# Optimization experiments

Hardware: AMD Instinct MI355X
Metric: run time of the kernel (lower is better)

The kernel has to match this reference:

```python
import jax, jax.numpy as jnp
import numpy as np

EMBED = 2048
N_HEAD = 32
N_KV = 8
HEAD_DIM = 64
GROUP = N_HEAD // N_KV


def _rope_tables(seq_len, head_dim):
    inv_freq = 1.0 / (10000.0 ** (jnp.arange(0, head_dim, 2, dtype=jnp.float32) / head_dim))
    ang = jnp.arange(seq_len, dtype=jnp.float32)[:, None] * inv_freq[None, :]  # [S, D/2]
    ang = jnp.concatenate([ang, ang], axis=-1)  # [S, D]
    return jnp.cos(ang), jnp.sin(ang)


def apply_rope(x, cos, sin, offset=0):
    # x: [B, H, S, D]
    S, D = x.shape[2], x.shape[3]
    x1, x2 = x[..., : D // 2], x[..., D // 2 :]
    c = cos[offset : offset + S][None, None]
    s = sin[offset : offset + S][None, None]
    rotated = jnp.concatenate([-x2, x1], axis=-1)
    return (x * c + rotated * s).astype(x.dtype)


def setup_inputs() -> dict:
    key = jax.random.key(0)
    kx, kq, kk, kv, ko = jax.random.split(key, 5)
    B, S = 2, 2048
    x = jax.random.normal(kx, (B, S, EMBED), dtype=jnp.float32)
    mask = jnp.triu(jnp.ones((S, S), dtype=bool), k=1)  # causal: True = masked
    cos, sin = _rope_tables(S, HEAD_DIM)
    std = 0.02
    Wq = jax.random.normal(kq, (EMBED, EMBED), dtype=jnp.float32) * std
    Wk = jax.random.normal(kk, (EMBED, N_KV * HEAD_DIM), dtype=jnp.float32) * std
    Wv = jax.random.normal(kv, (EMBED, N_KV * HEAD_DIM), dtype=jnp.float32) * std
    Wo = jax.random.normal(ko, (EMBED, EMBED), dtype=jnp.float32) * std
    return {"x": x, "mask": mask, "cos": cos, "sin": sin,
            "Wq": Wq, "Wk": Wk, "Wv": Wv, "Wo": Wo}


def reference(x, mask, cos, sin, Wq, Wk, Wv, Wo):
    B, S, E = x.shape
    # projections (no bias)
    q = (x @ Wq).reshape(B, S, N_HEAD, HEAD_DIM).transpose(0, 2, 1, 3)  # [B,H,S,D]
    k = (x @ Wk).reshape(B, S, N_KV, HEAD_DIM).transpose(0, 2, 1, 3)    # [B,G,S,D]
    v = (x @ Wv).reshape(B, S, N_KV, HEAD_DIM).transpose(0, 2, 1, 3)    # [B,G,S,D]
    q = apply_rope(q, cos, sin, offset=0)
    k = apply_rope(k, cos, sin, offset=0)
    next_k, next_v = k, v  # kv cache to return
    # GQA: head h uses kv group h // GROUP; avoid repeat_interleave via reshape
    qg = q.reshape(B, N_KV, GROUP, S, HEAD_DIM)
    scores = jnp.einsum('bgjsd,bgtd->bgjst', qg, k) / np.float32(np.sqrt(HEAD_DIM))
    scores = jnp.where(mask[None, None, None], -jnp.inf, scores)
    attn = jax.nn.softmax(scores, axis=-1)
    out = jnp.einsum('bgjst,bgtd->bgjsd', attn, v)          # [B,G,group,S,D]
    out = out.reshape(B, N_HEAD, S, HEAD_DIM).transpose(0, 2, 1, 3).reshape(B, S, E)
    return out @ Wo, next_k, next_v
```

## Files before the change

### kernel.cpp

```cpp
#include <hip/hip_runtime.h>
#include <hip/hip_bf16.h>
#include <math.h>

#define NH 32
#define NKV 8
#define HD 64
#define B_ 2
#define S_ 2048
#define E_ 2048
#define M_ 4096

typedef unsigned short ushort_t;
typedef __attribute__((ext_vector_type(8))) short short8;
typedef __attribute__((ext_vector_type(4))) short short4v;
typedef __attribute__((ext_vector_type(4))) float floatx4;

__device__ inline unsigned short f2bf(float f) {
  unsigned int u = __float_as_uint(f);
  return (unsigned short)((u + 0x7FFFu + ((u >> 16) & 1u)) >> 16);
}

__device__ inline float fexp2(float x) {
  float r;
  asm("v_exp_f32 %0, %1" : "=v"(r) : "v"(x));
  return r;
}

__device__ inline void ld_lds16(const void* g, void* l) {
  __builtin_amdgcn_global_load_lds((__attribute__((address_space(1))) void*)g,
                                   (__attribute__((address_space(3))) void*)l, 16, 0, 0);
}

__device__ inline void transp32(const float* __restrict__ in, ushort_t* __restrict__ out,
                                int R, int C, int bx, int by, int tid, float (*tile)[33]) {
  int c0 = bx * 32, r0 = by * 32;
  int x = tid & 31, y0 = tid >> 5;
  for (int i = 0; i < 4; i++) {
    int r = y0 + i * 8;
    tile[r][x] = in[(size_t)(r0 + r) * C + c0 + x];
  }
  __syncthreads();
  for (int i = 0; i < 4; i++) {
    int r = y0 + i * 8;
    out[(size_t)(c0 + r) * R + r0 + x] = f2bf(tile[x][r]);
  }
}

__global__ __launch_bounds__(256) void prep(const float* __restrict__ x,
                                            ushort_t* __restrict__ xb,
                                            const float* __restrict__ Wq,
                                            const float* __restrict__ Wk,
                                            const float* __restrict__ Wv,
                                            const float* __restrict__ Wo,
                                            ushort_t* __restrict__ WT,
                                            ushort_t* __restrict__ WoT) {
  __shared__ float tile[32][33];
  int bid = blockIdx.x, tid = threadIdx.x;
  if (bid < 4096) {
    size_t i = ((size_t)bid * 256 + tid) * 8;
    float4 a = *(const float4*)(x + i);
    float4 b = *(const float4*)(x + i + 4);
    short8 o;
    o[0] = (short)f2bf(a.x); o[1] = (short)f2bf(a.y);
    o[2] = (short)f2bf(a.z); o[3] = (short)f2bf(a.w);
    o[4] = (short)f2bf(b.x); o[5] = (short)f2bf(b.y);
    o[6] = (short)f2bf(b.z); o[7] = (short)f2bf(b.w);
    *(short8*)(xb + i) = o;
    return;
  }
  bid -= 4096;
  if (bid < 4096) { transp32(Wq, WT, 2048, 2048, bid & 63, bid >> 6, tid, tile); return; }
  bid -= 4096;
  if (bid < 1024) { transp32(Wk, WT + 2048 * 2048, 2048, 512, bid & 15, bid >> 4, tid, tile); return; }
  bid -= 1024;
  if (bid < 1024) { transp32(Wv, WT + 2560 * 2048, 2048, 512, bid & 15, bid >> 4, tid, tile); return; }
  bid -= 1024;
  transp32(Wo, WoT, 2048, 2048, bid & 63, bid >> 6, tid, tile);
}

__global__ __launch_bounds__(512) void gemm_qkv(const ushort_t* __restrict__ xb,
                                                const ushort_t* __restrict__ WT,
                                                ushort_t* __restrict__ qbf,
                                                float* __restrict__ outk,
                                                ushort_t* __restrict__ kbf,
                                                float* __restrict__ outv,
                                                ushort_t* __restrict__ vt,
                                                const float* __restrict__ cosP,
                                                const float* __restrict__ sinP) {
  __shared__ __align__(16) ushort_t L8[2][2][2][128][64];
  char* Lb = (char*)L8;
  int bid = blockIdx.x;
  int xcd = bid & 7, ii = bid >> 3;
  int mg = xcd >> 1, ng = xcd & 1;
  int m0 = (mg * 4 + ii / 6) * 256;
  int n0 = (ng * 6 + ii % 6) * 256;
  int tid = threadIdx.x;
  int w8 = tid >> 6, lane = tid & 63;
  int wrq = w8 >> 1, wcq = w8 & 1;
  int lr = lane & 15, quad = lane >> 4;
  int sx = lr & 7;
  int srow = w8 * 16 + (lane >> 3);
  int schunk = (lane & 7) ^ (lane >> 3);
  const char* abase = (const char*)(xb + (size_t)m0 * 2048);
  const char* bbase = (const char*)(WT + (size_t)n0 * 2048);
  floatx4 acc[4][2][4] = {};

#define STG(T, U)                                                                        \
  do {                                                                                   \
    const int mat_ = (U)&1, half_ = (U) >> 1;                                            \
    const char* sp = (mat_ ? bbase : abase) + (size_t)(half_ * 128 + srow) * 4096 +      \
                     (size_t)(T)*128 + schunk * 16;                                      \
    char* dp = Lb + (((T)&1) * 65536) + mat_ * 32768 + half_ * 16384 + w8 * 2048;        \
    ld_lds16(sp, dp);                                                                    \
    ld_lds16(sp + (size_t)8 * 4096, dp + 1024);                                          \
  } while (0)

#define PH(T, P, MH_, NH_, WAITS, DOSTAGE)                                               \
  do {                                                                                   \
    asm volatile(WAITS ::: "memory");                                                    \
    const char* Ab_ = Lb + (((T)&1) * 65536) + (MH_)*16384;                              \
    const char* Bb_ = Lb + (((T)&1) * 65536) + 32768 + (NH_)*16384;                      \
    short8 af_[2][2], bf_[4][2];                                                         \
    _Pragma("unroll") for (int i = 0; i < 2; i++) {                                      \
      size_t rb = (size_t)(wrq * 32 + i * 16 + lr) * 128;                                \
      _Pragma("unroll") for (int ks = 0; ks < 2; ks++)                                   \
          af_[i][ks] = *(const short8*)(Ab_ + rb + (((ks * 4 + quad) ^ sx) << 4));       \
    }                                                                                    \
    _Pragma("unroll") for (int j = 0; j < 4; j++) {                                      \
      size_t rb = (size_t)(wcq * 64 + j * 16 + lr) * 128;                                \
      _Pragma("unroll") for (int ks = 0; ks < 2; ks++)                                   \
          bf_[j][ks] = *(const short8*)(Bb_ + rb + (((ks * 4 + quad) ^ sx) << 4));       \
    }                                                                                    \
    if (DOSTAGE) STG((T) + 1, P);                                                        \
    __builtin_amdgcn_s_setprio(1);                                                       \
    _Pragma("unroll") for (int i = 0; i < 2; i++) _Pragma("unroll") for (int j = 0;      \
                                                                         j < 4; j++) {  \
      acc[P][i][j] =                                                                     \
          __builtin_amdgcn_mfma_f32_16x16x32_bf16(af_[i][0], bf_[j][0], acc[P][i][j],    \
                                                  0, 0, 0);                              \
      acc[P][i][j] =                                                                     \
          __builtin_amdgcn_mfma_f32_16x16x32_bf16(af_[i][1], bf_[j][1], acc[P][i][j],    \
                                                  0, 0, 0);                              \
    }                                                                                    \
    __builtin_amdgcn_s_setprio(0);                                                       \
  } while (0)

  STG(0, 0); STG(0, 1); STG(0, 2); STG(0, 3);

  for (int kt = 0; kt < 31; kt++) {
    PH(kt, 0, 0, 0, "s_waitcnt vmcnt(4)\n\ts_barrier", 1);
    PH(kt, 1, 1, 0, "s_waitcnt vmcnt(4)\n\ts_barrier", 1);
    PH(kt, 2, 1, 1, "s_waitcnt vmcnt(4)\n\ts_barrier", 1);
    PH(kt, 3, 0, 1, "s_barrier", 1);
  }
  PH(31, 0, 0, 0, "s_waitcnt vmcnt(4)\n\ts_barrier", 0);
  PH(31, 1, 1, 0, "s_waitcnt vmcnt(2)\n\ts_barrier", 0);
  PH(31, 2, 1, 1, "s_waitcnt vmcnt(0)\n\ts_barrier", 0);
  PH(31, 3, 0, 1, "s_barrier", 0);
#undef STG
#undef PH

  const int MHs[4] = {0, 1, 1, 0}, NHs[4] = {0, 0, 1, 1};
  if (n0 < 2048) {
    const float QS = 0.125f * 1.4426950408889634f;
#pragma unroll
    for (int p = 0; p < 4; p++)
#pragma unroll
      for (int i = 0; i < 2; i++)
#pragma unroll
        for (int j = 0; j < 2; j++) {
          int d = j * 16 + lr;
#pragma unroll
          for (int r = 0; r < 4; r++) {
            int row = m0 + MHs[p] * 128 + wrq * 32 + i * 16 + quad * 4 + r;
            int s = row & (S_ - 1);
            float c = cosP[s * 64 + d], sn = sinP[s * 64 + d];
            float x1 = acc[p][i][j][r], x2 = acc[p][i][j + 2][r];
            size_t oo = (size_t)row * 2048 + n0 + NHs[p] * 128 + wcq * 64 + d;
            qbf[oo] = f2bf((x1 * c - x2 * sn) * QS);
            qbf[oo + 32] = f2bf((x2 * c + x1 * sn) * QS);
          }
        }
  } else if (n0 < 2560) {
#pragma unroll
    for (int p = 0; p < 4; p++) {
      int h = ((n0 - 2048) >> 6) + NHs[p] * 2 + wcq;
#pragma unroll
      for (int i = 0; i < 2; i++)
#pragma unroll
        for (int j = 0; j < 2; j++) {
          int d = j * 16 + lr;
#pragma unroll
          for (int r = 0; r < 4; r++) {
            int row = m0 + MHs[p] * 128 + wrq * 32 + i * 16 + quad * 4 + r;
            int s = row & (S_ - 1), b = row >> 11;
            float c = cosP[s * 64 + d], sn = sinP[s * 64 + d];
            float x1 = acc[p][i][j][r], x2 = acc[p][i][j + 2][r];
            float y1 = x1 * c - x2 * sn, y2 = x2 * c + x1 * sn;
            size_t rowb = ((size_t)(b * NKV + h) * S_ + s) * 64;
            int xr = (s & 7) << 3;
            outk[rowb + d] = y1; outk[rowb + d + 32] = y2;
            kbf[rowb + (d ^ xr)] = f2bf(y1);
            kbf[rowb + ((d + 32) ^ xr)] = f2bf(y2);
          }
        }
    }
  } else {
#pragma unroll
    for (int p = 0; p < 4; p++) {
      int h = ((n0 - 2560) >> 6) + NHs[p] * 2 + wcq;
#pragma unroll
      for (int i = 0; i < 2; i++)
#pragma unroll
        for (int j = 0; j < 4; j++) {
          int d = j * 16 + lr;
          int row0 = m0 + MHs[p] * 128 + wrq * 32 + i * 16 + quad * 4;
          int s0 = row0 & (S_ - 1), b = row0 >> 11;
#pragma unroll
          for (int r = 0; r < 4; r++)
            outv[((size_t)(b * NKV + h) * S_ + s0 + r) * 64 + d] = acc[p][i][j][r];
          int tt = s0 >> 6, s4 = s0 & 63;
          short4v u;
          u[0] = (short)f2bf(acc[p][i][j][0]); u[1] = (short)f2bf(acc[p][i][j][1]);
          u[2] = (short)f2bf(acc[p][i][j][2]); u[3] = (short)f2bf(acc[p][i][j][3]);
          *(short4v*)(vt + ((size_t)(b * NKV + h) * 32 + tt) * 4096 + d * 64 +
                      (s4 ^ ((d & 7) << 3))) = u;
        }
    }
  }
}

__device__ __forceinline__ void gemm128_core(const ushort_t* __restrict__ Ag,
                                             const ushort_t* __restrict__ Bg,
                                             floatx4 (&acc)[4][4]) {
  __shared__ __align__(16) ushort_t As[2][128][64];
  __shared__ __align__(16) ushort_t Bs[2][128][64];
  int tid = threadIdx.x;
  int w = tid >> 6, lane = tid & 63;
  int wm = (w >> 1) * 64, wn = (w & 1) * 64;
  int lr = lane & 15, quad = lane >> 4;
  int sx = lr & 7;
  char* Asb = (char*)As;
  char* Bsb = (char*)Bs;

  size_t so[4];
#pragma unroll
  for (int s = 0; s < 4; s++)
    so[s] = (size_t)(w * 32 + s * 8 + (lane >> 3)) * 4096 + (size_t)(((lane & 7) ^ (lane >> 3)) * 16);
  const char* abase = (const char*)Ag;
  const char* bbase = (const char*)Bg;

#define STAGE128(buf, kt)                                          \
  do {                                                             \
    size_t ko = (size_t)(kt) * 128;                                \
    char* Ad = Asb + (buf) * 16384 + w * 4096;                     \
    char* Bd = Bsb + (buf) * 16384 + w * 4096;                     \
    _Pragma("unroll") for (int s = 0; s < 4; s++) {                \
      ld_lds16(abase + so[s] + ko, Ad + s * 1024);                 \
      ld_lds16(bbase + so[s] + ko, Bd + s * 1024);                 \
    }                                                              \
  } while (0)

  STAGE128(0, 0);
  __syncthreads();

  int cur = 0;
  for (int kt = 0; kt < 32; kt++) {
    if (kt < 31) STAGE128(cur ^ 1, kt + 1);
    const char* Ab = Asb + cur * 16384;
    const char* Bb = Bsb + cur * 16384;
    short8 af[4][2], bfr[4][2];
#pragma unroll
    for (int i = 0; i < 4; i++) {
      size_t rb = (size_t)(wm + i * 16 + lr) * 128;
#pragma unroll
      for (int ks = 0; ks < 2; ks++)
        af[i][ks] = *(const short8*)(Ab + rb + (((ks * 4 + quad) ^ sx) << 4));
    }
#pragma unroll
    for (int j = 0; j < 4; j++) {
      size_t rb = (size_t)(wn + j * 16 + lr) * 128;
#pragma unroll
      for (int ks = 0; ks < 2; ks++)
        bfr[j][ks] = *(const short8*)(Bb + rb + (((ks * 4 + quad) ^ sx) << 4));
    }
#pragma unroll
    for (int i = 0; i < 4; i++)
#pragma unroll
      for (int j = 0; j < 4; j++) {
        acc[i][j] = __builtin_amdgcn_mfma_f32_16x16x32_bf16(af[i][0], bfr[j][0], acc[i][j], 0, 0, 0);
        acc[i][j] = __builtin_amdgcn_mfma_f32_16x16x32_bf16(af[i][1], bfr[j][1], acc[i][j], 0, 0, 0);
      }
    __syncthreads();
    cur ^= 1;
  }
#undef STAGE128
}

__global__ __launch_bounds__(256) void gemm_o(const ushort_t* __restrict__ ctx,
                                              const ushort_t* __restrict__ WoT,
                                              float* __restrict__ y) {
  int o = blockIdx.y * 16 + blockIdx.x;
  int xcd = o & 7, i = o >> 3;
  int mg = xcd >> 1, ng = xcd & 1;
  int m0 = (mg * 8 + (i >> 3)) * 128;
  int n0 = (ng * 8 + (i & 7)) * 128;
  int tid = threadIdx.x;
  int w = tid >> 6, lane = tid & 63;
  int wm = (w >> 1) * 64, wn = (w & 1) * 64;
  int lr = lane & 15, quad = lane >> 4;

  floatx4 acc[4][4] = {};
  gemm128_core(ctx + (size_t)m0 * 2048, WoT + (size_t)n0 * 2048, acc);

#pragma unroll
  for (int i2 = 0; i2 < 4; i2++)
#pragma unroll
    for (int j = 0; j < 4; j++) {
      int row = m0 + wm + i2 * 16 + quad * 4;
      int col = n0 + wn + j * 16 + lr;
#pragma unroll
      for (int r = 0; r < 4; r++)
        y[(size_t)(row + r) * 2048 + col] = acc[i2][j][r];
    }
}

__global__ __launch_bounds__(256, 3) void attn2(ushort_t* __restrict__ q,
                                                const ushort_t* __restrict__ k,
                                                const ushort_t* __restrict__ vt) {
  __shared__ __align__(16) ushort_t KV[2][2][64][64];
  __shared__ __align__(16) ushort_t Ps[4][2][16][64];
  int bh = blockIdx.x;
  int qi = 15 - blockIdx.y;
  int b = bh >> 5, h = bh & 31, g = h >> 2;
  int tid = threadIdx.x;
  int w = tid >> 6, lane = tid & 63;
  int lr = lane & 15, quad = lane >> 4;

  int qg0 = qi * 128 + w * 16 + lr;
  int qg1 = qg0 + 64;
  short8 a00, a01, a10, a11;
  {
    const ushort_t* qp0 = q + ((size_t)(b * S_ + qg0) * NH + h) * HD;
    const ushort_t* qp1 = q + ((size_t)(b * S_ + qg1) * NH + h) * HD;
    a00 = *(const short8*)(qp0 + quad * 8);
    a01 = *(const short8*)(qp0 + 32 + quad * 8);
    a10 = *(const short8*)(qp1 + quad * 8);
    a11 = *(const short8*)(qp1 + 32 + quad * 8);
  }
  floatx4 od0[4] = {}, od1[4] = {};
  float mi0 = -INFINITY, li0 = 0.f, mi1 = -INFINITY, li1 = 0.f;

  const char* ksrc = (const char*)(k + (size_t)(b * NKV + g) * S_ * HD) + w * 2048 + lane * 16;
  const char* vsrc = (const char*)(vt + (size_t)(b * NKV + g) * S_ * HD) + w * 2048 + lane * 16;
  char* dB = (char*)&KV[0][0][0][0] + w * 2048;

  int sw = (lr & 7) << 4;
  int ro0 = (quad * 16) ^ sw;
  int ro1 = (64 + quad * 16) ^ sw;
  char* Pw = (char*)&Ps[0][0][0][0] + w * 4096;

  ld_lds16(ksrc, dB);
  ld_lds16(ksrc + 1024, dB + 1024);
  ld_lds16(vsrc, dB + 8192);
  ld_lds16(vsrc + 1024, dB + 8192 + 1024);
  asm volatile("s_waitcnt vmcnt(0)" ::: "memory");
  __syncthreads();

  int T = 2 * qi + 2;
  int cur = 0;
  for (int t = 0; t < T; t++) {
    if (t + 1 < T) {
      const char* kn = ksrc + (size_t)(t + 1) * 8192;
      const char* vn = vsrc + (size_t)(t + 1) * 8192;
      char* d = dB + (cur ^ 1) * 16384;
      ld_lds16(kn, d); ld_lds16(kn + 1024, d + 1024);
      ld_lds16(vn, d + 8192); ld_lds16(vn + 1024, d + 8192 + 1024);
    }
    const char* Kb = (const char*)&KV[cur][0][0][0];
    const char* Vb = (const char*)&KV[cur][1][0][0];
    bool dq0 = (t == 2 * qi);
    bool skip0 = (t == 2 * qi + 1);
    if (!skip0) {
      floatx4 sc[4];
      __builtin_amdgcn_s_setprio(1);
#pragma unroll
      for (int kn = 0; kn < 4; kn++) {
        short8 k0 = *(const short8*)(Kb + (kn * 16 + lr) * 128 + ro0);
        short8 k1 = *(const short8*)(Kb + (kn * 16 + lr) * 128 + ro1);
        floatx4 c = {};
        c = __builtin_amdgcn_mfma_f32_16x16x32_bf16(k0, a00, c, 0, 0, 0);
        c = __builtin_amdgcn_mfma_f32_16x16x32_bf16(k1, a01, c, 0, 0, 0);
        sc[kn] = c;
      }
      __builtin_amdgcn_s_setprio(0);
      float pv[16];
#pragma unroll
      for (int kn = 0; kn < 4; kn++)
#pragma unroll
        for (int r = 0; r < 4; r++) pv[kn * 4 + r] = sc[kn][r];
      if (dq0) {
#pragma unroll
        for (int e = 0; e < 16; e++) {
          int kg = t * 64 + (e >> 2) * 16 + quad * 4 + (e & 3);
          if (kg > qg0) pv[e] = -INFINITY;
        }
      }
      float mx = pv[0];
#pragma unroll
      for (int e = 1; e < 16; e++) mx = fmaxf(mx, pv[e]);
      mx = fmaxf(mx, __shfl_xor(mx, 16));
      mx = fmaxf(mx, __shfl_xor(mx, 32));
      if (__any(mx > mi0 + 11.5f)) {
        float mn = fmaxf(mi0, mx);
        float al = fexp2(mi0 - mn);
        li0 *= al;
#pragma unroll
        for (int dn = 0; dn < 4; dn++) {
          od0[dn][0] *= al; od0[dn][1] *= al; od0[dn][2] *= al; od0[dn][3] *= al;
        }
        mi0 = mn;
      }
      float ps = 0.f;
#pragma unroll
      for (int e = 0; e < 16; e++) {
        pv[e] = fexp2(pv[e] - mi0);
        ps += pv[e];
      }
      ps += __shfl_xor(ps, 16);
      ps += __shfl_xor(ps, 32);
      li0 += ps;
#pragma unroll
      for (int kn = 0; kn < 4; kn++) {
        unsigned int u0, u1;
        asm("v_cvt_pk_bf16_f32 %0, %1, %2" : "=v"(u0) : "v"(pv[kn * 4 + 0]), "v"(pv[kn * 4 + 1]));
        asm("v_cvt_pk_bf16_f32 %0, %1, %2" : "=v"(u1) : "v"(pv[kn * 4 + 2]), "v"(pv[kn * 4 + 3]));
        uint2 uu; uu.x = u0; uu.y = u1;
        *(uint2*)(Pw + lr * 128 + ((kn * 32 + quad * 8) ^ sw)) = uu;
      }
    }
    {
      floatx4 sc[4];
      __builtin_amdgcn_s_setprio(1);
#pragma unroll
      for (int kn = 0; kn < 4; kn++) {
        short8 k0 = *(const short8*)(Kb + (kn * 16 + lr) * 128 + ro0);
        short8 k1 = *(const short8*)(Kb + (kn * 16 + lr) * 128 + ro1);
        floatx4 c = {};
        c = __builtin_amdgcn_mfma_f32_16x16x32_bf16(k0, a10, c, 0, 0, 0);
        c = __builtin_amdgcn_mfma_f32_16x16x32_bf16(k1, a11, c, 0, 0, 0);
        sc[kn] = c;
      }
      __builtin_amdgcn_s_setprio(0);
      float pv[16];
#pragma unroll
      for (int kn = 0; kn < 4; kn++)
#pragma unroll
        for (int r = 0; r < 4; r++) pv[kn * 4 + r] = sc[kn][r];
      if (skip0) {
#pragma unroll
        for (int e = 0; e < 16; e++) {
          int kg = t * 64 + (e >> 2) * 16 + quad * 4 + (e & 3);
          if (kg > qg1) pv[e] = -INFINITY;
        }
      }
      float mx = pv[0];
#pragma unroll
      for (int e = 1; e < 16; e++) mx = fmaxf(mx, pv[e]);
      mx = fmaxf(mx, __shfl_xor(mx, 16));
      mx = fmaxf(mx, __shfl_xor(mx, 32));
      if (__any(mx > mi1 + 11.5f)) {
        float mn = fmaxf(mi1, mx);
        float al = fexp2(mi1 - mn);
        li1 *= al;
#pragma unroll
        for (int dn = 0; dn < 4; dn++) {
          od1[dn][0] *= al; od1[dn][1] *= al; od1[dn][2] *= al; od1[dn][3] *= al;
        }
        mi1 = mn;
      }
      float ps = 0.f;
#pragma unroll
      for (int e = 0; e < 16; e++) {
        pv[e] = fexp2(pv[e] - mi1);
        ps += pv[e];
      }
      ps += __shfl_xor(ps, 16);
      ps += __shfl_xor(ps, 32);
      li1 += ps;
#pragma unroll
      for (int kn = 0; kn < 4; kn++) {
        unsigned int u0, u1;
        asm("v_cvt_pk_bf16_f32 %0, %1, %2" : "=v"(u0) : "v"(pv[kn * 4 + 0]), "v"(pv[kn * 4 + 1]));
        asm("v_cvt_pk_bf16_f32 %0, %1, %2" : "=v"(u1) : "v"(pv[kn * 4 + 2]), "v"(pv[kn * 4 + 3]));
        uint2 uu; uu.x = u0; uu.y = u1;
        *(uint2*)(Pw + 2048 + lr * 128 + ((kn * 32 + quad * 8) ^ sw)) = uu;
      }
    }
    __builtin_amdgcn_s_setprio(1);
    if (!skip0) {
      short8 pb0 = *(const short8*)(Pw + lr * 128 + ro0);
      short8 pb1 = *(const short8*)(Pw + lr * 128 + ro1);
#pragma unroll
      for (int dn = 0; dn < 4; dn++) {
        short8 va = *(const short8*)(Vb + (dn * 16 + lr) * 128 + ro0);
        short8 vb = *(const short8*)(Vb + (dn * 16 + lr) * 128 + ro1);
        od0[dn] = __builtin_amdgcn_mfma_f32_16x16x32_bf16(va, pb0, od0[dn], 0, 0, 0);
        od0[dn] = __builtin_amdgcn_mfma_f32_16x16x32_bf16(vb, pb1, od0[dn], 0, 0, 0);
      }
    }
    {
      short8 pb0 = *(const short8*)(Pw + 2048 + lr * 128 + ro0);
      short8 pb1 = *(const short8*)(Pw + 2048 + lr * 128 + ro1);
#pragma unroll
      for (int dn = 0; dn < 4; dn++) {
        short8 va = *(const short8*)(Vb + (dn * 16 + lr) * 128 + ro0);
        short8 vb = *(const short8*)(Vb + (dn * 16 + lr) * 128 + ro1);
        od1[dn] = __builtin_amdgcn_mfma_f32_16x16x32_bf16(va, pb0, od1[dn], 0, 0, 0);
        od1[dn] = __builtin_amdgcn_mfma_f32_16x16x32_bf16(vb, pb1, od1[dn], 0, 0, 0);
      }
    }
    __builtin_amdgcn_s_setprio(0);
    asm volatile("s_waitcnt vmcnt(0)" ::: "memory");
    __syncthreads();
    cur ^= 1;
  }
  float inv0 = 1.f / li0, inv1 = 1.f / li1;
  ushort_t* outp0 = q + ((size_t)(b * S_ + qg0) * NH + h) * HD;
  ushort_t* outp1 = q + ((size_t)(b * S_ + qg1) * NH + h) * HD;
#pragma unroll
  for (int dn = 0; dn < 4; dn++) {
    short4v u;
    u[0] = (short)f2bf(od0[dn][0] * inv0); u[1] = (short)f2bf(od0[dn][1] * inv0);
    u[2] = (short)f2bf(od0[dn][2] * inv0); u[3] = (short)f2bf(od0[dn][3] * inv0);
    *(short4v*)(outp0 + dn * 16 + quad * 4) = u;
    short4v v;
    v[0] = (short)f2bf(od1[dn][0] * inv1); v[1] = (short)f2bf(od1[dn][1] * inv1);
    v[2] = (short)f2bf(od1[dn][2] * inv1); v[3] = (short)f2bf(od1[dn][3] * inv1);
    *(short4v*)(outp1 + dn * 16 + quad * 4) = v;
  }
}

extern "C" void kernel_launch(void* const* d_in, const int* in_sizes, int n_in,
                              void* d_out, int out_size, void* d_ws, size_t ws_size,
                              hipStream_t stream) {
  const float* x = (const float*)d_in[0];
  const float* cosT = (const float*)d_in[2];
  const float* sinT = (const float*)d_in[3];
  const float* Wq = (const float*)d_in[4];
  const float* Wk = (const float*)d_in[5];
  const float* Wv = (const float*)d_in[6];
  const float* Wo = (const float*)d_in[7];

  char* ws = (char*)d_ws;
  ushort_t* WT = (ushort_t*)(ws);
  ushort_t* WoT = (ushort_t*)(ws + 12582912);
  ushort_t* xb = (ushort_t*)(ws + 20971520);
  ushort_t* qbf = (ushort_t*)(ws + 37748736);
  ushort_t* kbf = (ushort_t*)(ws + 54525952);
  ushort_t* vt = (ushort_t*)(ws + 58720256);

  float* y = (float*)d_out;
  float* outk = y + (size_t)M_ * E_;
  float* outv = outk + (size_t)B_ * NKV * S_ * HD;

  prep<<<dim3(14336), 256, 0, stream>>>(x, xb, Wq, Wk, Wv, Wo, WT, WoT);

  gemm_qkv<<<dim3(192), 512, 0, stream>>>(xb, WT, qbf, outk, kbf, outv, vt, cosT, sinT);

  attn2<<<dim3(64, 16), 256, 0, stream>>>(qbf, kbf, vt);

  gemm_o<<<dim3(16, 32), 256, 0, stream>>>(qbf, WoT, y);
}
```

Measured before the change: 303.9 us.

## Restructure output GEMM into 128x256 tiles with 8 waves and phased pipelining

The output projection GEMM moves from 128x128 tiles with 4 waves to 128x256 tiles with 8 waves, launched as 256 blocks with an XCD-aware mapping. The K loop is split into four quadrant phases. Each phase loads one slice of the next tile through hand-placed vmcnt waits and barriers, raising MFMA priority with setprio so loads overlap compute. This aims to improve data reuse and latency hiding, at the cost of fewer blocks (256 on the GPU), a larger LDS footprint, and fragile manual waitcnt bookkeeping.

```diff
diff --git a/kernel.cpp b/kernel.cpp
--- a/kernel.cpp
+++ b/kernel.cpp
@@ -230,99 +230,106 @@
   }
 }
 
-__device__ __forceinline__ void gemm128_core(const ushort_t* __restrict__ Ag,
-                                             const ushort_t* __restrict__ Bg,
-                                             floatx4 (&acc)[4][4]) {
+__global__ __launch_bounds__(512) void gemm_o(const ushort_t* __restrict__ ctx,
+                                              const ushort_t* __restrict__ WoT,
+                                              float* __restrict__ y) {
   __shared__ __align__(16) ushort_t As[2][128][64];
-  __shared__ __align__(16) ushort_t Bs[2][128][64];
+  __shared__ __align__(16) ushort_t Bs[2][256][64];
+  char* Ab0 = (char*)As;
+  char* Bb0 = (char*)Bs;
+  int bid = blockIdx.x;
+  int xcd = bid & 7, ii = bid >> 3;
+  int mg = xcd >> 1, ng = xcd & 1;
+  int m0 = (mg * 8 + (ii >> 2)) * 128;
+  int n0 = (ng * 4 + (ii & 3)) * 256;
   int tid = threadIdx.x;
-  int w = tid >> 6, lane = tid & 63;
-  int wm = (w >> 1) * 64, wn = (w & 1) * 64;
+  int w8 = tid >> 6, lane = tid & 63;
+  int wrq = w8 >> 2, wcq = w8 & 3;
   int lr = lane & 15, quad = lane >> 4;
   int sx = lr & 7;
-  char* Asb = (char*)As;
-  char* Bsb = (char*)Bs;
-
-  size_t so[4];
-#pragma unroll
-  for (int s = 0; s < 4; s++)
-    so[s] = (size_t)(w * 32 + s * 8 + (lane >> 3)) * 4096 + (size_t)(((lane & 7) ^ (lane >> 3)) * 16);
-  const char* abase = (const char*)Ag;
-  const char* bbase = (const char*)Bg;
-
-#define STAGE128(buf, kt)                                          \
-  do {                                                             \
-    size_t ko = (size_t)(kt) * 128;                                \
-    char* Ad = Asb + (buf) * 16384 + w * 4096;                     \
-    char* Bd = Bsb + (buf) * 16384 + w * 4096;                     \
-    _Pragma("unroll") for (int s = 0; s < 4; s++) {                \
-      ld_lds16(abase + so[s] + ko, Ad + s * 1024);                 \
-      ld_lds16(bbase + so[s] + ko, Bd + s * 1024);                 \
-    }                                                              \
+  int lrow = lane >> 3;
+  int schunk = (lane & 7) ^ lrow;
+  const char* abase = (const char*)(ctx + (size_t)m0 * 2048);
+  const char* bbase = (const char*)(WoT + (size_t)n0 * 2048);
+  floatx4 acc[4][2][2] = {};
+
+#define STG_O(T, U)                                                                      \
+  do {                                                                                   \
+    size_t ko = (size_t)(T)*128;                                                         \
+    if (((U)&1) == 0) {                               \
+      const int half_ = (U) >> 1;                                                        \
+      const char* sp = abase + (size_t)(half_ * 64 + w8 * 8 + lrow) * 4096 + ko +        \
+                       schunk * 16;                                                      \
+      char* dp = Ab0 + (((T)&1) * 16384) + half_ * 8192 + w8 * 1024;                     \
+      ld_lds16(sp, dp);                                                                  \
+    } else {                                        \
+      const int half_ = (U) >> 1;                                                        \
+      const char* sp = bbase + (size_t)(half_ * 128 + w8 * 16 + lrow) * 4096 + ko +      \
+                       schunk * 16;                                                      \
+      char* dp = Bb0 + (((T)&1) * 32768) + half_ * 16384 + w8 * 2048;                    \
+      ld_lds16(sp, dp);                                                                  \
+      ld_lds16(sp + (size_t)8 * 4096, dp + 1024);                                        \
+    }                                                                                    \
   } while (0)
 
-  STAGE128(0, 0);
-  __syncthreads();
-
-  int cur = 0;
-  for (int kt = 0; kt < 32; kt++) {
-    if (kt < 31) STAGE128(cur ^ 1, kt + 1);
-    const char* Ab = Asb + cur * 16384;
-    const char* Bb = Bsb + cur * 16384;
-    short8 af[4][2], bfr[4][2];
-#pragma unroll
-    for (int i = 0; i < 4; i++) {
-      size_t rb = (size_t)(wm + i * 16 + lr) * 128;
-#pragma unroll
-      for (int ks = 0; ks < 2; ks++)
-        af[i][ks] = *(const short8*)(Ab + rb + (((ks * 4 + quad) ^ sx) << 4));
-    }
-#pragma unroll
-    for (int j = 0; j < 4; j++) {
-      size_t rb = (size_t)(wn + j * 16 + lr) * 128;
-#pragma unroll
-      for (int ks = 0; ks < 2; ks++)
-        bfr[j][ks] = *(const short8*)(Bb + rb + (((ks * 4 + quad) ^ sx) << 4));
-    }
-#pragma unroll
-    for (int i = 0; i < 4; i++)
-#pragma unroll
-      for (int j = 0; j < 4; j++) {
-        acc[i][j] = __builtin_amdgcn_mfma_f32_16x16x32_bf16(af[i][0], bfr[j][0], acc[i][j], 0, 0, 0);
-        acc[i][j] = __builtin_amdgcn_mfma_f32_16x16x32_bf16(af[i][1], bfr[j][1], acc[i][j], 0, 0, 0);
-      }
-    __syncthreads();
-    cur ^= 1;
-  }
-#undef STAGE128
-}
-
-__global__ __launch_bounds__(256) void gemm_o(const ushort_t* __restrict__ ctx,
-                                              const ushort_t* __restrict__ WoT,
-                                              float* __restrict__ y) {
-  int o = blockIdx.y * 16 + blockIdx.x;
-  int xcd = o & 7, i = o >> 3;
-  int mg = xcd >> 1, ng = xcd & 1;
-  int m0 = (mg * 8 + (i >> 3)) * 128;
-  int n0 = (ng * 8 + (i & 7)) * 128;
-  int tid = threadIdx.x;
-  int w = tid >> 6, lane = tid & 63;
-  int wm = (w >> 1) * 64, wn = (w & 1) * 64;
-  int lr = lane & 15, quad = lane >> 4;
-
-  floatx4 acc[4][4] = {};
-  gemm128_core(ctx + (size_t)m0 * 2048, WoT + (size_t)n0 * 2048, acc);
-
-#pragma unroll
-  for (int i2 = 0; i2 < 4; i2++)
-#pragma unroll
-    for (int j = 0; j < 4; j++) {
-      int row = m0 + wm + i2 * 16 + quad * 4;
-      int col = n0 + wn + j * 16 + lr;
-#pragma unroll
-      for (int r = 0; r < 4; r++)
-        y[(size_t)(row + r) * 2048 + col] = acc[i2][j][r];
-    }
+#define PH_O(T, P, MH_, NH_, WAITS, DOSTAGE)                                             \
+  do {                                                                                   \
+    asm volatile(WAITS ::: "memory");                                                    \
+    const char* Ab_ = Ab0 + (((T)&1) * 16384) + (MH_)*8192;                              \
+    const char* Bb_ = Bb0 + (((T)&1) * 32768) + (NH_)*16384;                             \
+    short8 af_[2][2], bf_[2][2];                                                         \
+    _Pragma("unroll") for (int i = 0; i < 2; i++) {                                      \
+      size_t rb = (size_t)(wrq * 32 + i * 16 + lr) * 128;                                \
+      _Pragma("unroll") for (int ks = 0; ks < 2; ks++)                                   \
+          af_[i][ks] = *(const short8*)(Ab_ + rb + (((ks * 4 + quad) ^ sx) << 4));       \
+    }                                                                                    \
+    _Pragma("unroll") for (int j = 0; j < 2; j++) {                                      \
+      size_t rb = (size_t)(wcq * 32 + j * 16 + lr) * 128;                                \
+      _Pragma("unroll") for (int ks = 0; ks < 2; ks++)                                   \
+          bf_[j][ks] = *(const short8*)(Bb_ + rb + (((ks * 4 + quad) ^ sx) << 4));       \
+    }                                                                                    \
+    if (DOSTAGE) STG_O((T) + 1, P);                                                      \
+    __builtin_amdgcn_s_setprio(1);                                                       \
+    _Pragma("unroll") for (int i = 0; i < 2; i++) _Pragma("unroll") for (int j = 0;      \
+                                                                         j < 2; j++) {  \
+      acc[P][i][j] =                                                                     \
+          __builtin_amdgcn_mfma_f32_16x16x32_bf16(af_[i][0], bf_[j][0], acc[P][i][j],    \
+                                                  0, 0, 0);                              \
+      acc[P][i][j] =                                                                     \
+          __builtin_amdgcn_mfma_f32_16x16x32_bf16(af_[i][1], bf_[j][1], acc[P][i][j],    \
+                                                  0, 0, 0);                              \
+    }                                                                                    \
+    __builtin_amdgcn_s_setprio(0);                                                       \
+  } while (0)
+
+  STG_O(0, 0); STG_O(0, 1); STG_O(0, 2); STG_O(0, 3);
+
+  for (int kt = 0; kt < 31; kt++) {
+    PH_O(kt, 0, 0, 0, "s_waitcnt vmcnt(3)\n\ts_barrier", 1);
+    PH_O(kt, 1, 1, 0, "s_waitcnt vmcnt(3)\n\ts_barrier", 1);
+    PH_O(kt, 2, 1, 1, "s_waitcnt vmcnt(3)\n\ts_barrier", 1);
+    PH_O(kt, 3, 0, 1, "s_barrier", 1);
+  }
+  PH_O(31, 0, 0, 0, "s_waitcnt vmcnt(3)\n\ts_barrier", 0);
+  PH_O(31, 1, 1, 0, "s_waitcnt vmcnt(2)\n\ts_barrier", 0);
+  PH_O(31, 2, 1, 1, "s_waitcnt vmcnt(0)\n\ts_barrier", 0);
+  PH_O(31, 3, 0, 1, "s_barrier", 0);
+#undef STG_O
+#undef PH_O
+
+  const int MHs[4] = {0, 1, 1, 0}, NHs[4] = {0, 0, 1, 1};
+#pragma unroll
+  for (int p = 0; p < 4; p++)
+#pragma unroll
+    for (int i = 0; i < 2; i++)
+#pragma unroll
+      for (int j = 0; j < 2; j++) {
+        int row = m0 + MHs[p] * 64 + wrq * 32 + i * 16 + quad * 4;
+        int col = n0 + NHs[p] * 128 + wcq * 32 + j * 16 + lr;
+#pragma unroll
+        for (int r = 0; r < 4; r++)
+          y[(size_t)(row + r) * 2048 + col] = acc[p][i][j][r];
+      }
 }
 
 __global__ __launch_bounds__(256, 3) void attn2(ushort_t* __restrict__ q,
@@ -570,5 +577,5 @@
 
   attn2<<<dim3(64, 16), 256, 0, stream>>>(qbf, kbf, vt);
 
-  gemm_o<<<dim3(16, 32), 256, 0, stream>>>(qbf, WoT, y);
-}
+  gemm_o<<<dim3(256), 512, 0, stream>>>(qbf, WoT, y);
+}
```

New measurement: 316.4 us. 4.1% more time.

## Move Wo transpose into attention launch and tree-reduce row max

Applied to the files above, without the earlier changes.

The Wo fp32-to-bf16 transpose moves out of the prep kernel and into extra trailing blocks of the attention launch, so that conversion can fill idle CUs during the attention tail instead of lengthening prep. The attention grid is flattened to 1D, with 1024 attention blocks followed by 4096 transpose blocks. The per-row max in the softmax also becomes a balanced tree of fmaxf, which shortens the dependency chain. In exchange, the attention kernel gains a 4KB shared tile, which could affect occupancy at launch_bounds(256,3).

```diff
diff --git a/kernel.cpp b/kernel.cpp
--- a/kernel.cpp
+++ b/kernel.cpp
@@ -51,9 +51,7 @@
                                             const float* __restrict__ Wq,
                                             const float* __restrict__ Wk,
                                             const float* __restrict__ Wv,
-                                            const float* __restrict__ Wo,
-                                            ushort_t* __restrict__ WT,
-                                            ushort_t* __restrict__ WoT) {
+                                            ushort_t* __restrict__ WT) {
   __shared__ float tile[32][33];
   int bid = blockIdx.x, tid = threadIdx.x;
   if (bid < 4096) {
@@ -73,9 +71,7 @@
   bid -= 4096;
   if (bid < 1024) { transp32(Wk, WT + 2048 * 2048, 2048, 512, bid & 15, bid >> 4, tid, tile); return; }
   bid -= 1024;
-  if (bid < 1024) { transp32(Wv, WT + 2560 * 2048, 2048, 512, bid & 15, bid >> 4, tid, tile); return; }
-  bid -= 1024;
-  transp32(Wo, WoT, 2048, 2048, bid & 63, bid >> 6, tid, tile);
+  transp32(Wv, WT + 2560 * 2048, 2048, 512, bid & 15, bid >> 4, tid, tile);
 }
 
 __global__ __launch_bounds__(512) void gemm_qkv(const ushort_t* __restrict__ xb,
@@ -327,13 +323,22 @@
 
 __global__ __launch_bounds__(256, 3) void attn2(ushort_t* __restrict__ q,
                                                 const ushort_t* __restrict__ k,
-                                                const ushort_t* __restrict__ vt) {
+                                                const ushort_t* __restrict__ vt,
+                                                const float* __restrict__ Wo,
+                                                ushort_t* __restrict__ WoT) {
   __shared__ __align__(16) ushort_t KV[2][2][64][64];
   __shared__ __align__(16) ushort_t Ps[4][2][16][64];
-  int bh = blockIdx.x;
-  int qi = 15 - blockIdx.y;
+  __shared__ float tile[32][33];
+  int bid0 = blockIdx.x;
+  int tid = threadIdx.x;
+  if (bid0 >= 1024) {
+    int bid2 = bid0 - 1024;
+    transp32(Wo, WoT, 2048, 2048, bid2 & 63, bid2 >> 6, tid, tile);
+    return;
+  }
+  int bh = bid0 & 63;
+  int qi = 15 - (bid0 >> 6);
   int b = bh >> 5, h = bh & 31, g = h >> 2;
-  int tid = threadIdx.x;
   int w = tid >> 6, lane = tid & 63;
   int lr = lane & 15, quad = lane >> 4;
 
@@ -406,9 +411,12 @@
           if (kg > qg0) pv[e] = -INFINITY;
         }
       }
-      float mx = pv[0];
-#pragma unroll
-      for (int e = 1; e < 16; e++) mx = fmaxf(mx, pv[e]);
+      float m01 = fmaxf(pv[0], pv[1]),  m23 = fmaxf(pv[2], pv[3]);
+      float m45 = fmaxf(pv[4], pv[5]),  m67 = fmaxf(pv[6], pv[7]);
+      float m89 = fmaxf(pv[8], pv[9]),  mab = fmaxf(pv[10], pv[11]);
+      float mcd = fmaxf(pv[12], pv[13]), mef = fmaxf(pv[14], pv[15]);
+      float mx = fmaxf(fmaxf(fmaxf(m01, m23), fmaxf(m45, m67)),
+                       fmaxf(fmaxf(m89, mab), fmaxf(mcd, mef)));
       mx = fmaxf(mx, __shfl_xor(mx, 16));
       mx = fmaxf(mx, __shfl_xor(mx, 32));
       if (__any(mx > mi0 + 11.5f)) {
@@ -464,9 +472,12 @@
           if (kg > qg1) pv[e] = -INFINITY;
         }
       }
-      float mx = pv[0];
-#pragma unroll
-      for (int e = 1; e < 16; e++) mx = fmaxf(mx, pv[e]);
+      float m01 = fmaxf(pv[0], pv[1]),  m23 = fmaxf(pv[2], pv[3]);
+      float m45 = fmaxf(pv[4], pv[5]),  m67 = fmaxf(pv[6], pv[7]);
+      float m89 = fmaxf(pv[8], pv[9]),  mab = fmaxf(pv[10], pv[11]);
+      float mcd = fmaxf(pv[12], pv[13]), mef = fmaxf(pv[14], pv[15]);
+      float mx = fmaxf(fmaxf(fmaxf(m01, m23), fmaxf(m45, m67)),
+                       fmaxf(fmaxf(m89, mab), fmaxf(mcd, mef)));
       mx = fmaxf(mx, __shfl_xor(mx, 16));
       mx = fmaxf(mx, __shfl_xor(mx, 32));
       if (__any(mx > mi1 + 11.5f)) {
@@ -564,11 +575,11 @@
   float* outk = y + (size_t)M_ * E_;
   float* outv = outk + (size_t)B_ * NKV * S_ * HD;
 
-  prep<<<dim3(14336), 256, 0, stream>>>(x, xb, Wq, Wk, Wv, Wo, WT, WoT);
+  prep<<<dim3(10240), 256, 0, stream>>>(x, xb, Wq, Wk, Wv, WT);
 
   gemm_qkv<<<dim3(192), 512, 0, stream>>>(xb, WT, qbf, outk, kbf, outv, vt, cosT, sinT);
 
-  attn2<<<dim3(64, 16), 256, 0, stream>>>(qbf, kbf, vt);
+  attn2<<<dim3(5120), 256, 0, stream>>>(qbf, kbf, vt, Wo, WoT);
 
   gemm_o<<<dim3(16, 32), 256, 0, stream>>>(qbf, WoT, y);
 }
```

Result: no change. 305.8 us (+0.6%).
